# Performance work log

Hardware: AMD Instinct MI355X
Metric: run time of the kernel (lower is better)

Reference implementation:

```python
import jax, jax.numpy as jnp
import numpy as np

B, HH, WW, C = 16, 56, 56, 384
HEADS, WS, SHIFT, HID = 12, 7, 3, 1536
N = WS * WS
EPS = 1e-5


def _rel_pos_index(ws):
    coords = np.stack(np.meshgrid(np.arange(ws), np.arange(ws), indexing='ij'))  # (2, ws, ws)
    cf = coords.reshape(2, -1)
    rel = (cf[:, :, None] - cf[:, None, :]).transpose(1, 2, 0).copy()  # (N, N, 2)
    rel[:, :, 0] += ws - 1
    rel[:, :, 1] += ws - 1
    rel[:, :, 0] *= 2 * ws - 1
    return rel.sum(-1)  # (N, N) int


def _attn_mask(H, W, ws, shift):
    img = np.zeros((H, W))
    sl = (slice(0, -ws), slice(-ws, -shift), slice(-shift, None))
    cnt = 0
    for h in sl:
        for w in sl:
            img[h, w] = cnt
            cnt += 1
    mw = img.reshape(H // ws, ws, W // ws, ws).transpose(0, 2, 1, 3).reshape(-1, ws * ws)  # (nW, N)
    am = mw[:, None, :] - mw[:, :, None]
    return np.where(am != 0, -100.0, 0.0).astype(np.float32)  # (nW, N, N)

REL_IDX = jnp.asarray(_rel_pos_index(WS))
ATTN_MASK = jnp.asarray(_attn_mask(HH, WW, WS, SHIFT))


def _ln(x, w, b):
    m = x.mean(-1, keepdims=True)
    v = ((x - m) ** 2).mean(-1, keepdims=True)
    return (x - m) * jax.lax.rsqrt(v + EPS) * w + b


def _win_part(x, ws):
    b, h, w, c = x.shape
    x = x.reshape(b, h // ws, ws, w // ws, ws, c).transpose(0, 1, 3, 2, 4, 5)
    return x.reshape(-1, ws * ws, c)


def _win_rev(wins, ws, h, w):
    c = wins.shape[-1]
    b = wins.shape[0] // ((h // ws) * (w // ws))
    x = wins.reshape(b, h // ws, w // ws, ws, ws, c).transpose(0, 1, 3, 2, 4, 5)
    return x.reshape(b, h, w, c)


def setup_inputs() -> dict:
    key = jax.random.key(0)
    ks = jax.random.split(key, 12)
    s = lambda fan: 1.0 / np.sqrt(fan)
    return {
        'x': jax.random.normal(ks[0], (B, HH * WW, C), jnp.float32),
        'norm1_w': jnp.ones((C,), jnp.float32),
        'norm1_b': jnp.zeros((C,), jnp.float32),
        'qkv_w': jax.random.normal(ks[1], (3 * C, C), jnp.float32) * s(C),
        'qkv_b': jnp.zeros((3 * C,), jnp.float32),
        'bias_table': jax.random.normal(ks[2], ((2 * WS - 1) ** 2, HEADS), jnp.float32) * 0.02,
        'proj_w': jax.random.normal(ks[3], (C, C), jnp.float32) * s(C),
        'proj_b': jnp.zeros((C,), jnp.float32),
        'norm2_w': jnp.ones((C,), jnp.float32),
        'norm2_b': jnp.zeros((C,), jnp.float32),
        'mlp_w1': jax.random.normal(ks[4], (HID, C), jnp.float32) * s(C),
        'mlp_b1': jnp.zeros((HID,), jnp.float32),
        'mlp_w2': jax.random.normal(ks[5], (C, HID), jnp.float32) * s(HID),
        'mlp_b2': jnp.zeros((C,), jnp.float32),
        'H': HH,
        'W': WW,
    }


def reference(x, norm1_w, norm1_b, qkv_w, qkv_b, bias_table, proj_w, proj_b,
              norm2_w, norm2_b, mlp_w1, mlp_b1, mlp_w2, mlp_b2, H, W):
    b = x.shape[0]
    shortcut = x
    h = _ln(x, norm1_w, norm1_b).reshape(b, H, W, C)
    # cyclic shift (H, W divisible by WS -> no padding needed)
    h = jnp.roll(h, shift=(-SHIFT, -SHIFT), axis=(1, 2))
    xw = _win_part(h, WS)  # (b*nW, N, C)
    Bw = xw.shape[0]
    hd = C // HEADS
    qkv = xw @ qkv_w.T + qkv_b  # (Bw, N, 3C)
    qkv = qkv.reshape(Bw, N, 3, HEADS, hd).transpose(2, 0, 3, 1, 4)
    q, k, v = qkv[0], qkv[1], qkv[2]  # (Bw, heads, N, hd)
    attn = jnp.einsum('bhnd,bhmd->bhnm', q * (hd ** -0.5), k)
    rel_bias = bias_table[REL_IDX.reshape(-1)].reshape(N, N, HEADS).transpose(2, 0, 1)
    attn = attn + rel_bias[None]
    nW = ATTN_MASK.shape[0]
    attn = attn.reshape(Bw // nW, nW, HEADS, N, N) + ATTN_MASK[None, :, None]
    attn = jax.nn.softmax(attn.reshape(Bw, HEADS, N, N), axis=-1)
    out = jnp.einsum('bhnm,bhmd->bhnd', attn, v).transpose(0, 2, 1, 3).reshape(Bw, N, C)
    out = out @ proj_w.T + proj_b
    h = _win_rev(out, WS, H, W)
    h = jnp.roll(h, shift=(SHIFT, SHIFT), axis=(1, 2)).reshape(b, H * W, C)
    x = shortcut + h
    y = _ln(x, norm2_w, norm2_b)
    y = jax.nn.gelu(y @ mlp_w1.T + mlp_b1, approximate=False) @ mlp_w2.T + mlp_b2
    return x + y
```

## Files before the change

### kernel.cpp

```cpp
#include <hip/hip_runtime.h>

typedef unsigned short ushort_t;
typedef __attribute__((ext_vector_type(8))) short bf16x8;
typedef __attribute__((ext_vector_type(4))) float f32x4;

__device__ __forceinline__ float b2f(ushort_t u) {
    union { float f; unsigned int u32; } x; x.u32 = ((unsigned int)u) << 16; return x.f;
}
__device__ __forceinline__ ushort_t f2b(float f) {
    union { float f; unsigned int u; } x; x.f = f;
    unsigned int r = x.u + 0x7fffu + ((x.u >> 16) & 1u);
    return (ushort_t)(r >> 16);
}
__device__ __forceinline__ float ldin(const void* p, size_t i, int fp32) {
    return fp32 ? ((const float*)p)[i] : b2f(((const ushort_t*)p)[i]);
}
__device__ __forceinline__ void gl_lds16(const ushort_t* g, ushort_t* l) {
    __builtin_amdgcn_global_load_lds((const __attribute__((address_space(1))) unsigned int*)g,
                                     (__attribute__((address_space(3))) unsigned int*)l, 16, 0, 0);
}
__device__ __forceinline__ float gelu_f(float x) {
    float xx = x * x;
    float u  = x * (0.7978845608028654f + 0.0356774081363f * xx);
    float a  = __builtin_fabsf(u);
    float e2 = __expf(-2.0f * a);
    float t  = (1.0f - e2) * __builtin_amdgcn_rcpf(1.0f + e2);
    t = __builtin_copysignf(t, u);
    return 0.5f * x * (1.0f + t);
}

struct Cv { const void* s; ushort_t* d; int n; };
struct CvA { Cv a[13]; };
__global__ void convert_all(CvA c, int total) {
    int fp32 = (*(const unsigned int*)c.a[0].s == 0x3F800000u);
    for (int idx = blockIdx.x * blockDim.x + threadIdx.x; idx < total; idx += gridDim.x * blockDim.x) {
        int i = idx, k = 0;
        while (k < 12 && i >= c.a[k].n) { i -= c.a[k].n; ++k; }
        c.a[k].d[i] = fp32 ? f2b(((const float*)c.a[k].s)[i]) : ((const ushort_t*)c.a[k].s)[i];
    }
}

__global__ __launch_bounds__(64) void ln_kernel(const void* __restrict__ x,
                                                const ushort_t* __restrict__ w,
                                                const ushort_t* __restrict__ bvec,
                                                ushort_t* __restrict__ out, int mode, int row_base,
                                                const void* __restrict__ flagsrc)
{
    int lr = blockIdx.x;
    int r = row_base + lr;
    int lane = threadIdx.x;
    int f32 = (mode == 1) ? 1 : (*(const unsigned int*)flagsrc == 0x3F800000u);
    long src;
    if (mode == 0) {
        int win = r / 49, pos = r % 49;
        int b = win >> 6, wy = (win >> 3) & 7, wx = win & 7;
        int py = pos / 7, px = pos - py * 7;
        int ys = wy * 7 + py + 3; if (ys >= 56) ys -= 56;
        int xs = wx * 7 + px + 3; if (xs >= 56) xs -= 56;
        src = (long)b * 3136 + ys * 56 + xs;
    } else {
        src = r;
    }
    float v[6];
    float s = 0.f, sq = 0.f;
#pragma unroll
    for (int j = 0; j < 6; ++j) {
        v[j] = ldin(x, src * 384 + lane + 64 * j, f32);
        s += v[j]; sq += v[j] * v[j];
    }
#pragma unroll
    for (int off = 32; off; off >>= 1) { s += __shfl_xor(s, off); sq += __shfl_xor(sq, off); }
    float mean = s * (1.f / 384.f);
    float var  = sq * (1.f / 384.f) - mean * mean;
    float rstd = rsqrtf(var + 1e-5f);
    ushort_t* op = out + (size_t)lr * 384;
#pragma unroll
    for (int j = 0; j < 6; ++j) {
        int c = lane + 64 * j;
        op[c] = f2b((v[j] - mean) * rstd * b2f(w[c]) + b2f(bvec[c]));
    }
}

__global__ __launch_bounds__(256) void attn_mfma(const ushort_t* __restrict__ qkv,
                                                 const ushort_t* __restrict__ bt,
                                                 ushort_t* __restrict__ out)
{
    __shared__ __align__(16) ushort_t Pb[4][64 * 72];
    __shared__ __align__(16) ushort_t Vb[4][32 * 72];
    int win = blockIdx.x;
    int t = threadIdx.x;
    int wave = t >> 6, lane = t & 63;
    int quad = lane >> 4, l16 = lane & 15;
    ushort_t* P  = Pb[wave];
    ushort_t* VT = Vb[wave];
    int wimg = win & 63;
    int wy = wimg >> 3, wx = wimg & 7;
    const float scale = 0.17677669529663687f;

    int rjv[4], cjv[4], gjv[4], cvalid[4];
#pragma unroll
    for (int jt = 0; jt < 4; ++jt) {
        int c = jt * 16 + l16;
        cvalid[jt] = (c < 49);
        int rj = c / 7, cj = c - rj * 7;
        rjv[jt] = rj; cjv[jt] = cj;
        int gjy = (wy == 7) ? (rj < 4 ? 1 : 2) : 0;
        int gjx = (wx == 7) ? (cj < 4 ? 1 : 2) : 0;
        gjv[jt] = gjy * 3 + gjx;
    }

    for (int hh = 0; hh < 3; ++hh) {
        int head = wave * 3 + hh;
        size_t base = (size_t)win * 49 * 1152 + (size_t)head * 32;

        bf16x8 qf[4], kf[4];
#pragma unroll
        for (int i = 0; i < 4; ++i) {
            int row = i * 16 + l16;
            bf16x8 z = {};
            qf[i] = z; kf[i] = z;
            if (row < 49) {
                qf[i] = *(const bf16x8*)(qkv + base + (size_t)row * 1152 + quad * 8);
                kf[i] = *(const bf16x8*)(qkv + base + (size_t)row * 1152 + 384 + quad * 8);
            }
        }
#pragma unroll
        for (int e = 0; e < 4; ++e) {
            int j = e * 16 + (lane >> 2);
            int db = (lane & 3) * 8;
            ushort_t buf[8] = {};
            if (j < 49) *(uint4*)buf = *(const uint4*)(qkv + base + (size_t)j * 1152 + 768 + db);
#pragma unroll
            for (int s = 0; s < 8; ++s) VT[(db + s) * 72 + j] = buf[s];
        }

        f32x4 Sv[4][4];
#pragma unroll
        for (int i = 0; i < 4; ++i)
#pragma unroll
            for (int j = 0; j < 4; ++j) {
                f32x4 z = {};
                Sv[i][j] = __builtin_amdgcn_mfma_f32_16x16x32_bf16(qf[i], kf[j], z, 0, 0, 0);
            }

#pragma unroll
        for (int it = 0; it < 4; ++it) {
#pragma unroll
            for (int r = 0; r < 4; ++r) {
                int m = it * 16 + quad * 4 + r;
                int ri = m / 7, ci = m - ri * 7;
                int giy = (wy == 7) ? (ri < 4 ? 1 : 2) : 0;
                int gix = (wx == 7) ? (ci < 4 ? 1 : 2) : 0;
                int gi = giy * 3 + gix;
                float vals[4];
                float vmax = -1e30f;
#pragma unroll
                for (int jt = 0; jt < 4; ++jt) {
                    float sv = -1e30f;
                    if (m < 49 && cvalid[jt]) {
                        int rel = (ri - rjv[jt] + 6) * 13 + (ci - cjv[jt] + 6);
                        sv = Sv[it][jt][r] * scale + b2f(bt[rel * 12 + head]);
                        if (gi != gjv[jt]) sv -= 100.f;
                    }
                    vals[jt] = sv;
                    vmax = fmaxf(vmax, sv);
                }
#pragma unroll
                for (int off = 1; off < 16; off <<= 1) vmax = fmaxf(vmax, __shfl_xor(vmax, off));
                float ssum = 0.f;
#pragma unroll
                for (int jt = 0; jt < 4; ++jt) { float e = __expf(vals[jt] - vmax); vals[jt] = e; ssum += e; }
#pragma unroll
                for (int off = 1; off < 16; off <<= 1) ssum += __shfl_xor(ssum, off);
                float inv = __builtin_amdgcn_rcpf(ssum);
#pragma unroll
                for (int jt = 0; jt < 4; ++jt) P[m * 72 + jt * 16 + l16] = f2b(vals[jt] * inv);
            }
        }

        f32x4 Ov[4][2] = {};
#pragma unroll
        for (int kk = 0; kk < 2; ++kk) {
            bf16x8 vb[2];
            vb[0] = *(const bf16x8*)&VT[(l16) * 72 + kk * 32 + quad * 8];
            vb[1] = *(const bf16x8*)&VT[(16 + l16) * 72 + kk * 32 + quad * 8];
#pragma unroll
            for (int mt = 0; mt < 4; ++mt) {
                bf16x8 pa = *(const bf16x8*)&P[(mt * 16 + l16) * 72 + kk * 32 + quad * 8];
                Ov[mt][0] = __builtin_amdgcn_mfma_f32_16x16x32_bf16(pa, vb[0], Ov[mt][0], 0, 0, 0);
                Ov[mt][1] = __builtin_amdgcn_mfma_f32_16x16x32_bf16(pa, vb[1], Ov[mt][1], 0, 0, 0);
            }
        }
#pragma unroll
        for (int mt = 0; mt < 4; ++mt)
#pragma unroll
            for (int r = 0; r < 4; ++r) {
                int m = mt * 16 + quad * 4 + r;
                if (m < 49) {
                    size_t orow = ((size_t)win * 49 + m) * 384 + (size_t)head * 32;
                    out[orow + l16]      = f2b(Ov[mt][0][r]);
                    out[orow + 16 + l16] = f2b(Ov[mt][1][r]);
                }
            }
    }
}

template <int EPI>
__global__ __launch_bounds__(256) void gemm_k(const ushort_t* __restrict__ A,
                                              const ushort_t* __restrict__ Bw,
                                              const ushort_t* __restrict__ bias,
                                              const void* __restrict__ residv,
                                              void* __restrict__ outv,
                                              int N, int K, long rbase,
                                              const void* __restrict__ flagsrc)
{
    __shared__ __align__(16) ushort_t lA[128 * 32];
    __shared__ __align__(16) ushort_t lB[128 * 32];
    int m0 = blockIdx.y * 128, n0 = blockIdx.x * 128;
    int t = threadIdx.x;
    int wave = t >> 6, lane = t & 63;
    int quad = lane >> 4, l16 = lane & 15;
    int wrow = (wave >> 1) * 64, wcol = (wave & 1) * 64;
    f32x4 acc[4][4] = {};

    int srow = wave * 32 + (lane >> 2);
    int scol = (lane & 3) * 8;
    const ushort_t* gA0 = A  + (size_t)(m0 + srow) * K + scol;
    const ushort_t* gA1 = gA0 + (size_t)16 * K;
    const ushort_t* gB0 = Bw + (size_t)(n0 + srow) * K + scol;
    const ushort_t* gB1 = gB0 + (size_t)16 * K;
    ushort_t* lA0 = &lA[wave * 1024];
    ushort_t* lA1 = &lA[wave * 1024 + 512];
    ushort_t* lB0 = &lB[wave * 1024];
    ushort_t* lB1 = &lB[wave * 1024 + 512];

    for (int k0 = 0; k0 < K; k0 += 32) {
        __syncthreads();
        gl_lds16(gA0 + k0, lA0);
        gl_lds16(gA1 + k0, lA1);
        gl_lds16(gB0 + k0, lB0);
        gl_lds16(gB1 + k0, lB1);
        __syncthreads();
        bf16x8 af[4], bf[4];
#pragma unroll
        for (int i = 0; i < 4; ++i)
            af[i] = *(const bf16x8*)(&lA[(wrow + i * 16 + l16) * 32 + quad * 8]);
#pragma unroll
        for (int j = 0; j < 4; ++j)
            bf[j] = *(const bf16x8*)(&lB[(wcol + j * 16 + l16) * 32 + quad * 8]);
#pragma unroll
        for (int i = 0; i < 4; ++i)
#pragma unroll
            for (int j = 0; j < 4; ++j)
                acc[i][j] = __builtin_amdgcn_mfma_f32_16x16x32_bf16(af[i], bf[j], acc[i][j], 0, 0, 0);
    }

    float bb[4];
#pragma unroll
    for (int j = 0; j < 4; ++j) bb[j] = b2f(bias[n0 + wcol + j * 16 + l16]);
    int rf32 = (EPI == 2) ? (*(const unsigned int*)flagsrc == 0x3F800000u) : 1;

#pragma unroll
    for (int i = 0; i < 4; ++i) {
#pragma unroll
        for (int rix = 0; rix < 4; ++rix) {
            int m = m0 + wrow + i * 16 + quad * 4 + rix;
            unsigned orow = 0;
            if (EPI == 2) {
                int mg = (int)rbase + m;
                int win = mg / 49, pos = mg - win * 49;
                int b = win >> 6, wy = (win >> 3) & 7, wx = win & 7;
                int py = pos / 7, px = pos - py * 7;
                int y = wy * 7 + py + 3; if (y >= 56) y -= 56;
                int x = wx * 7 + px + 3; if (x >= 56) x -= 56;
                orow = (unsigned)(b * 3136 + y * 56 + x);
            } else if (EPI == 3) {
                orow = (unsigned)(rbase + m);
            }
#pragma unroll
            for (int j = 0; j < 4; ++j) {
                int n = n0 + wcol + j * 16 + l16;
                float vv = acc[i][j][rix] + bb[j];
                if (EPI == 0) {
                    ((ushort_t*)outv)[(unsigned)m * (unsigned)N + (unsigned)n] = f2b(vv);
                } else if (EPI == 1) {
                    ((ushort_t*)outv)[(unsigned)m * (unsigned)N + (unsigned)n] = f2b(gelu_f(vv));
                } else {
                    float r = ldin(residv, (size_t)orow * 384 + n, rf32);
                    ((float*)outv)[(size_t)orow * 384 + n] = vv + r;
                }
            }
        }
    }
}

extern "C" void kernel_launch(void* const* d_in, const int* in_sizes, int n_in,
                              void* d_out, int out_size, void* d_ws, size_t ws_size,
                              hipStream_t stream)
{
    (void)in_sizes; (void)n_in; (void)out_size;
    char* ws = (char*)d_ws;
    size_t off = 0;
    auto alloc = [&](size_t bytes) { size_t p = off; off = (off + bytes + 255) & ~(size_t)255; return p; };

    size_t o_n1w  = alloc(384 * 2);
    size_t o_n1b  = alloc(384 * 2);
    size_t o_qw   = alloc(442368ull * 2);
    size_t o_qb   = alloc(1152 * 2);
    size_t o_bt   = alloc(2028 * 2);
    size_t o_pw   = alloc(147456ull * 2);
    size_t o_pb   = alloc(384 * 2);
    size_t o_n2w  = alloc(384 * 2);
    size_t o_n2b  = alloc(384 * 2);
    size_t o_w1   = alloc(589824ull * 2);
    size_t o_b1   = alloc(1536 * 2);
    size_t o_w2   = alloc(589824ull * 2);
    size_t o_b2   = alloc(384 * 2);

    size_t avail = (ws_size > off) ? ws_size - off : 0;
    int M_c;
    if      (avail >= (size_t)50176 * 3840 + 1024) M_c = 50176;
    else if (avail >= (size_t)12544 * 3840 + 1024) M_c = 12544;
    else                                            M_c = 6272;
    int nch = 50176 / M_c;
    size_t o_s1 = alloc((size_t)M_c * 768);
    size_t o_s2 = alloc((size_t)M_c * 3072);

    ushort_t* n1w  = (ushort_t*)(ws + o_n1w);
    ushort_t* n1b  = (ushort_t*)(ws + o_n1b);
    ushort_t* qw   = (ushort_t*)(ws + o_qw);
    ushort_t* qb   = (ushort_t*)(ws + o_qb);
    ushort_t* bt   = (ushort_t*)(ws + o_bt);
    ushort_t* pw   = (ushort_t*)(ws + o_pw);
    ushort_t* pb   = (ushort_t*)(ws + o_pb);
    ushort_t* n2w  = (ushort_t*)(ws + o_n2w);
    ushort_t* n2b  = (ushort_t*)(ws + o_n2b);
    ushort_t* w1   = (ushort_t*)(ws + o_w1);
    ushort_t* b1   = (ushort_t*)(ws + o_b1);
    ushort_t* w2   = (ushort_t*)(ws + o_w2);
    ushort_t* b2v  = (ushort_t*)(ws + o_b2);
    ushort_t* s1   = (ushort_t*)(ws + o_s1);
    ushort_t* s2   = (ushort_t*)(ws + o_s2);
    const void* x  = d_in[0];
    const void* fs = d_in[1];
    float* xmid    = (float*)d_out;

    CvA ca;
    ca.a[0]  = {d_in[1],  n1w, 384};
    ca.a[1]  = {d_in[2],  n1b, 384};
    ca.a[2]  = {d_in[3],  qw,  442368};
    ca.a[3]  = {d_in[4],  qb,  1152};
    ca.a[4]  = {d_in[5],  bt,  2028};
    ca.a[5]  = {d_in[6],  pw,  147456};
    ca.a[6]  = {d_in[7],  pb,  384};
    ca.a[7]  = {d_in[8],  n2w, 384};
    ca.a[8]  = {d_in[9],  n2b, 384};
    ca.a[9]  = {d_in[10], w1,  589824};
    ca.a[10] = {d_in[11], b1,  1536};
    ca.a[11] = {d_in[12], w2,  589824};
    ca.a[12] = {d_in[13], b2v, 384};
    convert_all<<<2048, 256, 0, stream>>>(ca, 1776492);

    for (int c = 0; c < nch; ++c) {
        int rb = c * M_c;
        ln_kernel<<<dim3(M_c), dim3(64), 0, stream>>>(x, n1w, n1b, s1, 0, rb, fs);
        gemm_k<0><<<dim3(9, M_c / 128), dim3(256), 0, stream>>>(s1, qw, qb, nullptr, s2, 1152, 384, 0, fs);
        attn_mfma<<<dim3(M_c / 49), dim3(256), 0, stream>>>(s2, bt, s1);
        gemm_k<2><<<dim3(3, M_c / 128), dim3(256), 0, stream>>>(s1, pw, pb, x, xmid, 384, 384, rb, fs);
    }
    for (int c = 0; c < nch; ++c) {
        int rb = c * M_c;
        ln_kernel<<<dim3(M_c), dim3(64), 0, stream>>>(xmid, n2w, n2b, s1, 1, rb, fs);
        gemm_k<1><<<dim3(12, M_c / 128), dim3(256), 0, stream>>>(s1, w1, b1, nullptr, s2, 1536, 384, 0, fs);
        gemm_k<3><<<dim3(3, M_c / 128), dim3(256), 0, stream>>>(s2, w2, b2v, xmid, (float*)d_out, 384, 1536, rb, fs);
    }
}
```

Measured before the change: 685.8 us.

## Double-buffer GEMM LDS with swizzled layout and pack four LN rows per block

The GEMM now stages the next K-tile into a second LDS buffer while computing on the current one, which cuts the two barriers per step down to one. LDS reads use an XOR swizzle, matched by permuting the global source columns, to reduce bank conflicts. The LayerNorm kernel now processes four rows per 256-thread block instead of one row per 64-thread block, to reduce block launch overhead. Doubling LDS may lower occupancy.

```diff
diff --git a/kernel.cpp b/kernel.cpp
--- a/kernel.cpp
+++ b/kernel.cpp
@@ -40,15 +40,15 @@
     }
 }
 
-__global__ __launch_bounds__(64) void ln_kernel(const void* __restrict__ x,
-                                                const ushort_t* __restrict__ w,
-                                                const ushort_t* __restrict__ bvec,
-                                                ushort_t* __restrict__ out, int mode, int row_base,
-                                                const void* __restrict__ flagsrc)
+__global__ __launch_bounds__(256) void ln_kernel(const void* __restrict__ x,
+                                                 const ushort_t* __restrict__ w,
+                                                 const ushort_t* __restrict__ bvec,
+                                                 ushort_t* __restrict__ out, int mode, int row_base,
+                                                 const void* __restrict__ flagsrc)
 {
-    int lr = blockIdx.x;
+    int wave = threadIdx.x >> 6, lane = threadIdx.x & 63;
+    int lr = blockIdx.x * 4 + wave;
     int r = row_base + lr;
-    int lane = threadIdx.x;
     int f32 = (mode == 1) ? 1 : (*(const unsigned int*)flagsrc == 0x3F800000u);
     long src;
     if (mode == 0) {
@@ -214,8 +214,8 @@
                                               int N, int K, long rbase,
                                               const void* __restrict__ flagsrc)
 {
-    __shared__ __align__(16) ushort_t lA[128 * 32];
-    __shared__ __align__(16) ushort_t lB[128 * 32];
+    __shared__ __align__(16) ushort_t lA[2][128 * 32];
+    __shared__ __align__(16) ushort_t lB[2][128 * 32];
     int m0 = blockIdx.y * 128, n0 = blockIdx.x * 128;
     int t = threadIdx.x;
     int wave = t >> 6, lane = t & 63;
@@ -224,35 +224,41 @@
     f32x4 acc[4][4] = {};
 
     int srow = wave * 32 + (lane >> 2);
-    int scol = (lane & 3) * 8;
+    int fsw  = (srow >> 1) & 3;
+    int scol = (((lane & 3) ^ fsw)) * 8;
     const ushort_t* gA0 = A  + (size_t)(m0 + srow) * K + scol;
     const ushort_t* gA1 = gA0 + (size_t)16 * K;
     const ushort_t* gB0 = Bw + (size_t)(n0 + srow) * K + scol;
     const ushort_t* gB1 = gB0 + (size_t)16 * K;
-    ushort_t* lA0 = &lA[wave * 1024];
-    ushort_t* lA1 = &lA[wave * 1024 + 512];
-    ushort_t* lB0 = &lB[wave * 1024];
-    ushort_t* lB1 = &lB[wave * 1024 + 512];
-
+
+    auto stage = [&](int buf, int k0) {
+        gl_lds16(gA0 + k0, &lA[buf][wave * 1024]);
+        gl_lds16(gA1 + k0, &lA[buf][wave * 1024 + 512]);
+        gl_lds16(gB0 + k0, &lB[buf][wave * 1024]);
+        gl_lds16(gB1 + k0, &lB[buf][wave * 1024 + 512]);
+    };
+
+    stage(0, 0);
+    __syncthreads();
+
+    int sl = (quad ^ ((l16 >> 1) & 3)) * 8;
+    int cur = 0;
     for (int k0 = 0; k0 < K; k0 += 32) {
-        __syncthreads();
-        gl_lds16(gA0 + k0, lA0);
-        gl_lds16(gA1 + k0, lA1);
-        gl_lds16(gB0 + k0, lB0);
-        gl_lds16(gB1 + k0, lB1);
-        __syncthreads();
+        if (k0 + 32 < K) stage(cur ^ 1, k0 + 32);
         bf16x8 af[4], bf[4];
 #pragma unroll
         for (int i = 0; i < 4; ++i)
-            af[i] = *(const bf16x8*)(&lA[(wrow + i * 16 + l16) * 32 + quad * 8]);
+            af[i] = *(const bf16x8*)(&lA[cur][(wrow + i * 16 + l16) * 32 + sl]);
 #pragma unroll
         for (int j = 0; j < 4; ++j)
-            bf[j] = *(const bf16x8*)(&lB[(wcol + j * 16 + l16) * 32 + quad * 8]);
+            bf[j] = *(const bf16x8*)(&lB[cur][(wcol + j * 16 + l16) * 32 + sl]);
 #pragma unroll
         for (int i = 0; i < 4; ++i)
 #pragma unroll
             for (int j = 0; j < 4; ++j)
                 acc[i][j] = __builtin_amdgcn_mfma_f32_16x16x32_bf16(af[i], bf[j], acc[i][j], 0, 0, 0);
+        __syncthreads();
+        cur ^= 1;
     }
 
     float bb[4];
@@ -363,14 +369,14 @@
 
     for (int c = 0; c < nch; ++c) {
         int rb = c * M_c;
-        ln_kernel<<<dim3(M_c), dim3(64), 0, stream>>>(x, n1w, n1b, s1, 0, rb, fs);
+        ln_kernel<<<dim3(M_c / 4), dim3(256), 0, stream>>>(x, n1w, n1b, s1, 0, rb, fs);
         gemm_k<0><<<dim3(9, M_c / 128), dim3(256), 0, stream>>>(s1, qw, qb, nullptr, s2, 1152, 384, 0, fs);
         attn_mfma<<<dim3(M_c / 49), dim3(256), 0, stream>>>(s2, bt, s1);
         gemm_k<2><<<dim3(3, M_c / 128), dim3(256), 0, stream>>>(s1, pw, pb, x, xmid, 384, 384, rb, fs);
     }
     for (int c = 0; c < nch; ++c) {
         int rb = c * M_c;
-        ln_kernel<<<dim3(M_c), dim3(64), 0, stream>>>(xmid, n2w, n2b, s1, 1, rb, fs);
+        ln_kernel<<<dim3(M_c / 4), dim3(256), 0, stream>>>(xmid, n2w, n2b, s1, 1, rb, fs);
         gemm_k<1><<<dim3(12, M_c / 128), dim3(256), 0, stream>>>(s1, w1, b1, nullptr, s2, 1536, 384, 0, fs);
         gemm_k<3><<<dim3(3, M_c / 128), dim3(256), 0, stream>>>(s2, w2, b2v, xmid, (float*)d_out, 384, 1536, rb, fs);
     }
```

Result: faster. 667.3 us (-2.7%).
